# Kernel optimization log

Measured on AMD Instinct MI355X. Metric: run time of the kernel, lower is better.

Reference implementation:

```python
import jax, jax.numpy as jnp
import numpy as np

B, C, H, W = 4, 256, 64, 64
HEADS = 4
GROUPS = 32
EPS = 1e-5


def setup_inputs() -> dict:
    key = jax.random.key(0)
    k1, k2, k3 = jax.random.split(key, 3)
    x = jax.random.normal(k1, (B, C, H, W), dtype=jnp.float32)
    gn_weight = jnp.ones((C,), dtype=jnp.float32)
    gn_bias = jnp.zeros((C,), dtype=jnp.float32)
    qkv_w = jax.random.normal(k2, (3 * C, C), dtype=jnp.float32) / np.sqrt(C)
    qkv_b = jnp.zeros((3 * C,), dtype=jnp.float32)
    proj_w = jax.random.normal(k3, (C, C), dtype=jnp.float32) / np.sqrt(C)
    proj_b = jnp.zeros((C,), dtype=jnp.float32)
    return {"x": x, "gn_weight": gn_weight, "gn_bias": gn_bias,
            "qkv_w": qkv_w, "qkv_b": qkv_b, "proj_w": proj_w, "proj_b": proj_b}


def _group_norm(x, weight, bias):
    b, c, h, w = x.shape
    xg = x.reshape(b, GROUPS, c // GROUPS, h * w)
    mean = jnp.mean(xg, axis=(2, 3), keepdims=True)
    var = jnp.var(xg, axis=(2, 3), keepdims=True)
    xg = (xg - mean) * jax.lax.rsqrt(var + EPS)
    xn = xg.reshape(b, c, h, w)
    return xn * weight[None, :, None, None] + bias[None, :, None, None]


def reference(x, gn_weight, gn_bias, qkv_w, qkv_b, proj_w, proj_b):
    b, c, h, w = x.shape
    t = h * w
    residual = x
    xn = _group_norm(x, gn_weight, gn_bias).reshape(b, c, t)
    # conv1x1 == matmul over channel dim
    qkv = jnp.einsum('oc,bct->bot', qkv_w, xn) + qkv_b[None, :, None]
    q, k, v = jnp.split(qkv, 3, axis=1)
    d = c // HEADS
    q = q.reshape(b * HEADS, d, t)
    k = k.reshape(b * HEADS, d, t)
    v = v.reshape(b * HEADS, d, t)
    scale = 1.0 / np.sqrt(d)
    weight = jnp.einsum('bct,bcs->bts', q * scale, k)  # [b*heads, t, t]
    weight = jax.nn.softmax(weight.astype(jnp.float32), axis=-1).astype(q.dtype)
    a = jnp.einsum('bts,bcs->bct', weight, v).reshape(b, c, t)
    a = jnp.einsum('oc,bct->bot', proj_w, a) + proj_b[None, :, None]
    return a.reshape(b, c, h, w) + residual
```

## Files before the change

### kernel.cpp

```cpp
#include <hip/hip_runtime.h>
#include <hip/hip_bf16.h>

#define NB 4
#define NC 256
#define NT 4096
#define NHEADS 4
#define DHD 64
#define NBH 16
#define NGROUPS 32
#define CPG 8
#define GN_EPS 1e-5f

typedef __attribute__((ext_vector_type(4))) float f32x4;
typedef __attribute__((ext_vector_type(8))) short s16x8;
typedef __attribute__((ext_vector_type(4))) short s16x4;

__device__ __forceinline__ unsigned short f2bf(float f) {
  union { float f; unsigned int u; } v; v.f = f;
  return (unsigned short)((v.u + 0x7fffu + ((v.u >> 16) & 1u)) >> 16);
}

__global__ __launch_bounds__(256) void k_cvt_w(const float* __restrict__ qkv_w,
                                               const float* __restrict__ proj_w,
                                               unsigned short* __restrict__ wq,
                                               unsigned short* __restrict__ wp) {
  int i = blockIdx.x * 256 + threadIdx.x;
  if (i < 768 * 256) wq[i] = f2bf(qkv_w[i]);
  if (i < 256 * 256) wp[i] = f2bf(proj_w[i]);
}

__global__ __launch_bounds__(256) void k_gn(const float* __restrict__ x,
                                            const float* __restrict__ gw,
                                            const float* __restrict__ gb,
                                            unsigned short* __restrict__ xnT) {
  int b = blockIdx.x >> 5;
  int g = blockIdx.x & 31;
  const float* xp = x + ((size_t)(b * NC + g * CPG)) * NT;
  int tid = threadIdx.x;
  float s = 0.f, ss = 0.f;
  const f32x4* xp4 = (const f32x4*)xp;
  for (int i = tid; i < (CPG * NT) / 4; i += 256) {
    f32x4 v = xp4[i];
    s += v.x + v.y + v.z + v.w;
    ss += v.x * v.x + v.y * v.y + v.z * v.z + v.w * v.w;
  }
#pragma unroll
  for (int off = 32; off > 0; off >>= 1) {
    s += __shfl_down(s, off);
    ss += __shfl_down(ss, off);
  }
  __shared__ float red[8];
  int w = tid >> 6;
  if ((tid & 63) == 0) { red[w * 2] = s; red[w * 2 + 1] = ss; }
  __syncthreads();
  float stot = red[0] + red[2] + red[4] + red[6];
  float sstot = red[1] + red[3] + red[5] + red[7];
  float mean = stot * (1.f / 32768.f);
  float var = sstot * (1.f / 32768.f) - mean * mean;
  float rstd = rsqrtf(var + GN_EPS);
  float sc[CPG], sh[CPG];
#pragma unroll
  for (int j = 0; j < CPG; ++j) {
    float gsc = rstd * gw[g * CPG + j];
    sc[j] = gsc;
    sh[j] = gb[g * CPG + j] - mean * gsc;
  }
  for (int t = tid; t < NT; t += 256) {
    s16x8 o;
#pragma unroll
    for (int j = 0; j < CPG; ++j)
      o[j] = (short)f2bf(fmaf(xp[(size_t)j * NT + t], sc[j], sh[j]));
    *(s16x8*)(xnT + ((size_t)b * NT + t) * NC + g * CPG) = o;
  }
}

__global__ __launch_bounds__(256) void k_qkv(const unsigned short* __restrict__ wq,
                                             const float* __restrict__ qkv_b,
                                             const unsigned short* __restrict__ xnT,
                                             unsigned short* __restrict__ qT,
                                             unsigned short* __restrict__ kT,
                                             unsigned short* __restrict__ vS) {
  int wid = blockIdx.x * 4 + (threadIdx.x >> 6);
  int lane = threadIdx.x & 63;
  int l15 = lane & 15, lg = lane >> 4;
  int b = wid / (48 * 256);
  int rem = wid - b * (48 * 256);
  int ot = rem >> 8, tt = rem & 255;
  f32x4 acc = {0.f, 0.f, 0.f, 0.f};
  const unsigned short* arow = wq + (size_t)(ot * 16 + l15) * NC;
  const unsigned short* brow = xnT + ((size_t)b * NT + tt * 16 + l15) * NC;
#pragma unroll
  for (int kk = 0; kk < 8; ++kk) {
    int c0 = kk * 32 + lg * 8;
    s16x8 af = *(const s16x8*)(arow + c0);
    s16x8 bf = *(const s16x8*)(brow + c0);
    acc = __builtin_amdgcn_mfma_f32_16x16x32_bf16(af, bf, acc, 0, 0, 0);
  }
  int o0 = ot * 16 + lg * 4;
  int t = tt * 16 + l15;
  float r0 = acc[0] + qkv_b[o0 + 0];
  float r1 = acc[1] + qkv_b[o0 + 1];
  float r2 = acc[2] + qkv_b[o0 + 2];
  float r3 = acc[3] + qkv_b[o0 + 3];
  int which = o0 >> 8;
  int cc = o0 & 255;
  int h = cc >> 6, d0 = cc & 63;
  int bh = b * NHEADS + h;
  if (which == 0) {
    s16x4 pk = {(short)f2bf(r0 * 0.125f), (short)f2bf(r1 * 0.125f),
                (short)f2bf(r2 * 0.125f), (short)f2bf(r3 * 0.125f)};
    *(s16x4*)(qT + ((size_t)bh * NT + t) * DHD + d0) = pk;
  } else if (which == 1) {
    s16x4 pk = {(short)f2bf(r0), (short)f2bf(r1), (short)f2bf(r2), (short)f2bf(r3)};
    *(s16x4*)(kT + ((size_t)bh * NT + t) * DHD + d0) = pk;
  } else {
    vS[((size_t)bh * DHD + d0 + 0) * NT + t] = f2bf(r0);
    vS[((size_t)bh * DHD + d0 + 1) * NT + t] = f2bf(r1);
    vS[((size_t)bh * DHD + d0 + 2) * NT + t] = f2bf(r2);
    vS[((size_t)bh * DHD + d0 + 3) * NT + t] = f2bf(r3);
  }
}

__global__ __launch_bounds__(256) void k_attn(const unsigned short* __restrict__ qT,
                                              const unsigned short* __restrict__ kT,
                                              const unsigned short* __restrict__ vS,
                                              unsigned short* __restrict__ aT) {
  int wid = blockIdx.x * 4 + (threadIdx.x >> 6);
  int lane = threadIdx.x & 63;
  int l15 = lane & 15, lg = lane >> 4;
  int bh = wid >> 7;
  int tq0 = (wid & 127) << 5;
  s16x8 qf[2][2];
#pragma unroll
  for (int tt = 0; tt < 2; ++tt)
#pragma unroll
    for (int kk = 0; kk < 2; ++kk)
      qf[tt][kk] = *(const s16x8*)(qT + ((size_t)bh * NT + tq0 + tt * 16 + l15) * DHD + kk * 32 + lg * 8);
  f32x4 O[2][4];
#pragma unroll
  for (int tt = 0; tt < 2; ++tt)
#pragma unroll
    for (int d = 0; d < 4; ++d) O[tt][d] = (f32x4){0.f, 0.f, 0.f, 0.f};
  float mx[2] = {-1e30f, -1e30f};
  float ls[2] = {0.f, 0.f};
  for (int s0 = 0; s0 < NT; s0 += 16) {
    const unsigned short* krow = kT + ((size_t)bh * NT + s0 + l15) * DHD + lg * 8;
    s16x8 kf0 = *(const s16x8*)(krow);
    s16x8 kf1 = *(const s16x8*)(krow + 32);
    s16x4 vf[4];
#pragma unroll
    for (int dblk = 0; dblk < 4; ++dblk)
      vf[dblk] = *(const s16x4*)(vS + ((size_t)bh * DHD + dblk * 16 + l15) * NT + s0 + lg * 4);
#pragma unroll
    for (int tt = 0; tt < 2; ++tt) {
      f32x4 st = {0.f, 0.f, 0.f, 0.f};
      st = __builtin_amdgcn_mfma_f32_16x16x32_bf16(kf0, qf[tt][0], st, 0, 0, 0);
      st = __builtin_amdgcn_mfma_f32_16x16x32_bf16(kf1, qf[tt][1], st, 0, 0, 0);
      float tmax = fmaxf(fmaxf(st[0], st[1]), fmaxf(st[2], st[3]));
      tmax = fmaxf(tmax, __shfl_xor(tmax, 16));
      tmax = fmaxf(tmax, __shfl_xor(tmax, 32));
      float mn = fmaxf(mx[tt], tmax);
      float corr = __expf(mx[tt] - mn);
      mx[tt] = mn;
      float p0 = __expf(st[0] - mn);
      float p1 = __expf(st[1] - mn);
      float p2 = __expf(st[2] - mn);
      float p3 = __expf(st[3] - mn);
      float psum = p0 + p1 + p2 + p3;
      psum += __shfl_xor(psum, 16);
      psum += __shfl_xor(psum, 32);
      ls[tt] = ls[tt] * corr + psum;
      s16x4 pf = {(short)f2bf(p0), (short)f2bf(p1), (short)f2bf(p2), (short)f2bf(p3)};
#pragma unroll
      for (int dblk = 0; dblk < 4; ++dblk) {
        O[tt][dblk] = O[tt][dblk] * corr;
        O[tt][dblk] = __builtin_amdgcn_mfma_f32_16x16x16bf16_1k(vf[dblk], pf, O[tt][dblk], 0, 0, 0);
      }
    }
  }
  int b = bh >> 2, h = bh & 3;
#pragma unroll
  for (int tt = 0; tt < 2; ++tt) {
    float inv = 1.0f / ls[tt];
    int t = tq0 + tt * 16 + l15;
#pragma unroll
    for (int dblk = 0; dblk < 4; ++dblk) {
      s16x4 pk;
#pragma unroll
      for (int r = 0; r < 4; ++r) pk[r] = (short)f2bf(O[tt][dblk][r] * inv);
      *(s16x4*)(aT + ((size_t)b * NT + t) * NC + h * DHD + dblk * 16 + lg * 4) = pk;
    }
  }
}

__global__ __launch_bounds__(256) void k_proj(const unsigned short* __restrict__ wp,
                                              const float* __restrict__ proj_b,
                                              const unsigned short* __restrict__ aT,
                                              const float* __restrict__ x,
                                              float* __restrict__ out) {
  int wid = blockIdx.x * 4 + (threadIdx.x >> 6);
  int lane = threadIdx.x & 63;
  int l15 = lane & 15, lg = lane >> 4;
  int b = wid / (16 * 256);
  int rem = wid - b * (16 * 256);
  int ot = rem >> 8, tt = rem & 255;
  f32x4 acc = {0.f, 0.f, 0.f, 0.f};
  const unsigned short* arow = wp + (size_t)(ot * 16 + l15) * NC;
  const unsigned short* brow = aT + ((size_t)b * NT + tt * 16 + l15) * NC;
#pragma unroll
  for (int kk = 0; kk < 8; ++kk) {
    int c0 = kk * 32 + lg * 8;
    s16x8 af = *(const s16x8*)(arow + c0);
    s16x8 bf = *(const s16x8*)(brow + c0);
    acc = __builtin_amdgcn_mfma_f32_16x16x32_bf16(af, bf, acc, 0, 0, 0);
  }
  int c0 = ot * 16 + lg * 4;
  int t = tt * 16 + l15;
#pragma unroll
  for (int r = 0; r < 4; ++r) {
    int c = c0 + r;
    size_t idx = ((size_t)b * NC + c) * NT + t;
    out[idx] = acc[r] + proj_b[c] + x[idx];
  }
}

extern "C" void kernel_launch(void* const* d_in, const int* in_sizes, int n_in,
                              void* d_out, int out_size, void* d_ws, size_t ws_size,
                              hipStream_t stream) {
  const float* x      = (const float*)d_in[0];
  const float* gw     = (const float*)d_in[1];
  const float* gb     = (const float*)d_in[2];
  const float* qkv_w  = (const float*)d_in[3];
  const float* qkv_b  = (const float*)d_in[4];
  const float* proj_w = (const float*)d_in[5];
  const float* proj_b = (const float*)d_in[6];
  float* out = (float*)d_out;
  char* ws = (char*)d_ws;
  unsigned short* xnT = (unsigned short*)(ws);
  unsigned short* aT  = (unsigned short*)(ws);
  unsigned short* qT  = (unsigned short*)(ws + (8u  << 20));
  unsigned short* kT  = (unsigned short*)(ws + (16u << 20));
  unsigned short* vS  = (unsigned short*)(ws + (24u << 20));
  unsigned short* wqb = (unsigned short*)(ws + (32u << 20));
  unsigned short* wpb = (unsigned short*)(ws + (32u << 20) + 768 * 256 * 2);

  hipLaunchKernelGGL(k_cvt_w, dim3(768), dim3(256), 0, stream, qkv_w, proj_w, wqb, wpb);
  hipLaunchKernelGGL(k_gn, dim3(128), dim3(256), 0, stream, x, gw, gb, xnT);
  hipLaunchKernelGGL(k_qkv, dim3(12288), dim3(256), 0, stream, wqb, qkv_b, xnT, qT, kT, vS);
  hipLaunchKernelGGL(k_attn, dim3(512), dim3(256), 0, stream, qT, kT, vS, aT);
  hipLaunchKernelGGL(k_proj, dim3(4096), dim3(256), 0, stream, wpb, proj_b, aT, x, out);
}
```

Baseline: 558.2 us.

## Process 64-key tiles with exp2 softmax, lazy rescaling, and packed bf16 conversion

Folds log2(e) into the query scale so the softmax can use the native exp2 instruction. The attention loop now handles 64 keys per iteration instead of 16, which cuts per-step shuffles and max reductions. The running max and output are rescaled only when the new max exceeds the old one by more than 8, and probabilities are converted with the hardware packed bf16 instruction. The larger tile raises register pressure, and the lazy rescale lets unnormalized values grow, but with a threshold of 8 that stays bounded.

New measurement: 562.3 us. About the same (+0.7%).

```diff
diff --git a/kernel.cpp b/kernel.cpp
--- a/kernel.cpp
+++ b/kernel.cpp
@@ -107,8 +107,9 @@
   int h = cc >> 6, d0 = cc & 63;
   int bh = b * NHEADS + h;
   if (which == 0) {
-    s16x4 pk = {(short)f2bf(r0 * 0.125f), (short)f2bf(r1 * 0.125f),
-                (short)f2bf(r2 * 0.125f), (short)f2bf(r3 * 0.125f)};
+    const float qs = 0.125f * 1.4426950408889634f;
+    s16x4 pk = {(short)f2bf(r0 * qs), (short)f2bf(r1 * qs),
+                (short)f2bf(r2 * qs), (short)f2bf(r3 * qs)};
     *(s16x4*)(qT + ((size_t)bh * NT + t) * DHD + d0) = pk;
   } else if (which == 1) {
     s16x4 pk = {(short)f2bf(r0), (short)f2bf(r1), (short)f2bf(r2), (short)f2bf(r3)};
@@ -143,39 +144,76 @@
     for (int d = 0; d < 4; ++d) O[tt][d] = (f32x4){0.f, 0.f, 0.f, 0.f};
   float mx[2] = {-1e30f, -1e30f};
   float ls[2] = {0.f, 0.f};
-  for (int s0 = 0; s0 < NT; s0 += 16) {
-    const unsigned short* krow = kT + ((size_t)bh * NT + s0 + l15) * DHD + lg * 8;
-    s16x8 kf0 = *(const s16x8*)(krow);
-    s16x8 kf1 = *(const s16x8*)(krow + 32);
-    s16x4 vf[4];
+  const unsigned short* kbase0 = kT + ((size_t)bh * NT + l15) * DHD + lg * 8;
+  const unsigned short* vbase0 = vS + (size_t)bh * DHD * NT + 4 * lg;
+  for (int s0 = 0; s0 < NT; s0 += 64) {
+    const unsigned short* kbase = kbase0 + (size_t)s0 * DHD;
+    s16x8 kf[4][2];
+#pragma unroll
+    for (int sub = 0; sub < 4; ++sub) {
+      kf[sub][0] = *(const s16x8*)(kbase + sub * 16 * DHD);
+      kf[sub][1] = *(const s16x8*)(kbase + sub * 16 * DHD + 32);
+    }
+    s16x4 vf[4][4];
 #pragma unroll
     for (int dblk = 0; dblk < 4; ++dblk)
-      vf[dblk] = *(const s16x4*)(vS + ((size_t)bh * DHD + dblk * 16 + l15) * NT + s0 + lg * 4);
+#pragma unroll
+      for (int sub = 0; sub < 4; ++sub)
+        vf[dblk][sub] = *(const s16x4*)(vbase0 + (size_t)(dblk * 16 + l15) * NT + s0 + sub * 16);
 #pragma unroll
     for (int tt = 0; tt < 2; ++tt) {
-      f32x4 st = {0.f, 0.f, 0.f, 0.f};
-      st = __builtin_amdgcn_mfma_f32_16x16x32_bf16(kf0, qf[tt][0], st, 0, 0, 0);
-      st = __builtin_amdgcn_mfma_f32_16x16x32_bf16(kf1, qf[tt][1], st, 0, 0, 0);
-      float tmax = fmaxf(fmaxf(st[0], st[1]), fmaxf(st[2], st[3]));
-      tmax = fmaxf(tmax, __shfl_xor(tmax, 16));
-      tmax = fmaxf(tmax, __shfl_xor(tmax, 32));
-      float mn = fmaxf(mx[tt], tmax);
-      float corr = __expf(mx[tt] - mn);
-      mx[tt] = mn;
-      float p0 = __expf(st[0] - mn);
-      float p1 = __expf(st[1] - mn);
-      float p2 = __expf(st[2] - mn);
-      float p3 = __expf(st[3] - mn);
-      float psum = p0 + p1 + p2 + p3;
+      f32x4 st[4];
+#pragma unroll
+      for (int sub = 0; sub < 4; ++sub) {
+        f32x4 z = {0.f, 0.f, 0.f, 0.f};
+        z = __builtin_amdgcn_mfma_f32_16x16x32_bf16(kf[sub][0], qf[tt][0], z, 0, 0, 0);
+        z = __builtin_amdgcn_mfma_f32_16x16x32_bf16(kf[sub][1], qf[tt][1], z, 0, 0, 0);
+        st[sub] = z;
+      }
+      float tm01 = fmaxf(fmaxf(st[0][0], st[0][1]), fmaxf(st[0][2], st[0][3]));
+      float tm02 = fmaxf(fmaxf(st[1][0], st[1][1]), fmaxf(st[1][2], st[1][3]));
+      float tm03 = fmaxf(fmaxf(st[2][0], st[2][1]), fmaxf(st[2][2], st[2][3]));
+      float tm04 = fmaxf(fmaxf(st[3][0], st[3][1]), fmaxf(st[3][2], st[3][3]));
+      float tm = fmaxf(fmaxf(tm01, tm02), fmaxf(tm03, tm04));
+      tm = fmaxf(tm, __shfl_xor(tm, 16));
+      tm = fmaxf(tm, __shfl_xor(tm, 32));
+      if (!__all(tm <= mx[tt] + 8.f)) {
+        float mnew = fmaxf(mx[tt], tm);
+        float corr = __builtin_amdgcn_exp2f(mx[tt] - mnew);
+        mx[tt] = mnew;
+        ls[tt] *= corr;
+#pragma unroll
+        for (int d = 0; d < 4; ++d) O[tt][d] *= corr;
+      }
+      float m = mx[tt];
+      f32x4 pv4[4];
+      float psum = 0.f;
+#pragma unroll
+      for (int sub = 0; sub < 4; ++sub)
+#pragma unroll
+        for (int r = 0; r < 4; ++r) {
+          float e = __builtin_amdgcn_exp2f(st[sub][r] - m);
+          pv4[sub][r] = e;
+          psum += e;
+        }
       psum += __shfl_xor(psum, 16);
       psum += __shfl_xor(psum, 32);
-      ls[tt] = ls[tt] * corr + psum;
-      s16x4 pf = {(short)f2bf(p0), (short)f2bf(p1), (short)f2bf(p2), (short)f2bf(p3)};
-#pragma unroll
-      for (int dblk = 0; dblk < 4; ++dblk) {
-        O[tt][dblk] = O[tt][dblk] * corr;
-        O[tt][dblk] = __builtin_amdgcn_mfma_f32_16x16x16bf16_1k(vf[dblk], pf, O[tt][dblk], 0, 0, 0);
+      ls[tt] += psum;
+      s16x4 pf[4];
+#pragma unroll
+      for (int sub = 0; sub < 4; ++sub) {
+        unsigned int pk01, pk23;
+        asm("v_cvt_pk_bf16_f32 %0, %1, %2" : "=v"(pk01) : "v"(pv4[sub][0]), "v"(pv4[sub][1]));
+        asm("v_cvt_pk_bf16_f32 %0, %1, %2" : "=v"(pk23) : "v"(pv4[sub][2]), "v"(pv4[sub][3]));
+        union { unsigned int u[2]; s16x4 v; } pu;
+        pu.u[0] = pk01; pu.u[1] = pk23;
+        pf[sub] = pu.v;
       }
+#pragma unroll
+      for (int dblk = 0; dblk < 4; ++dblk)
+#pragma unroll
+        for (int sub = 0; sub < 4; ++sub)
+          O[tt][dblk] = __builtin_amdgcn_mfma_f32_16x16x16bf16_1k(vf[dblk][sub], pf[sub], O[tt][dblk], 0, 0, 0);
     }
   }
   int b = bh >> 2, h = bh & 3;
```
